# Kernel optimization log

Hardware: AMD Instinct MI355X
Metric: run time of the kernel (lower is better)

The kernel has to match this reference:

```python
import jax, jax.numpy as jnp
import numpy as np

B, T, NT = 256, 1024, 96  # batch, max seq len, num_tags (incl. start/end)


def setup_inputs() -> dict:
    key = jax.random.key(0)
    k1, k2, k3 = jax.random.split(key, 3)
    h = jax.random.normal(k1, (B, T, NT), dtype=jnp.float32)
    # lengths in [1, T]; force at least one full-length sequence so max_len == T
    lengths = jax.random.randint(k2, (B,), 1, T + 1).at[0].set(T)
    trans = jax.random.normal(k3, (NT, NT), dtype=jnp.float32)  # trans[to, from]
    return {"h": h, "lengths": lengths, "trans": trans}


def reference(h, lengths, trans):
    # CRF forward algorithm (log partition function), masked for variable lengths.
    Bb, Tt, nt = h.shape
    start_tag, end_tag = nt - 2, nt - 1  # start_tag=-2, end_tag=-1
    mask = jnp.arange(Tt)[None, :] < lengths[:, None]  # [B, T]

    score0 = jnp.full((Bb, nt), -10000.0, dtype=h.dtype).at[:, start_tag].set(0.0)

    def step(score, xs):
        h_t, m_t = xs  # h_t: [B, NT], m_t: [B]
        # score[b, j] (prev tag j) + trans[i, j] + emit h_t[b, i] -> [B, NT(i), NT(j)]
        s = score[:, None, :] + trans[None, :, :] + h_t[:, :, None]
        s = jax.nn.logsumexp(s, axis=2)  # [B, NT]
        score = jnp.where(m_t[:, None], s, score)
        return score, None

    score, _ = jax.lax.scan(step, score0, (jnp.swapaxes(h, 0, 1), mask.T))
    # transition into end tag, then final logsumexp over tags -> [B]
    return jax.nn.logsumexp(score + trans[end_tag][None, :], axis=1)
```

## Files before the change

### kernel.cpp

```cpp
#include <hip/hip_runtime.h>

#define Bb 256
#define Tt 1024
#define NT 96
#define PF 8

__global__ __attribute__((amdgpu_flat_work_group_size(256, 256),
                          amdgpu_waves_per_eu(1, 1)))
void crf_fwd_kernel(
    const float* __restrict__ h,
    const int*   __restrict__ lengths,
    const float* __restrict__ trans,
    float* __restrict__ out)
{
    const int b    = blockIdx.x;
    const int tid  = threadIdx.x;
    const int i    = tid >> 1;
    const int q    = tid & 1;
    const int L    = lengths[b];
    const bool active = (i < NT);
    const int wave = tid >> 6;

    __shared__ float p_lds[2][128];
    __shared__ float fin[4];

    float E[48];
    {
        const int ic = active ? i : 0;
        const float4* tr4 = reinterpret_cast<const float4*>(trans + ic * NT + q * 48);
        #pragma unroll
        for (int m = 0; m < 12; ++m) {
            const float4 t4 = tr4[m];
            E[4*m+0] = __expf(t4.x);
            E[4*m+1] = __expf(t4.y);
            E[4*m+2] = __expf(t4.z);
            E[4*m+3] = __expf(t4.w);
        }
    }
    asm volatile("" : "+v"(E[0]),  "+v"(E[1]),  "+v"(E[2]),  "+v"(E[3]),
                      "+v"(E[4]),  "+v"(E[5]),  "+v"(E[6]),  "+v"(E[7]),
                      "+v"(E[8]),  "+v"(E[9]),  "+v"(E[10]), "+v"(E[11]));
    asm volatile("" : "+v"(E[12]), "+v"(E[13]), "+v"(E[14]), "+v"(E[15]),
                      "+v"(E[16]), "+v"(E[17]), "+v"(E[18]), "+v"(E[19]),
                      "+v"(E[20]), "+v"(E[21]), "+v"(E[22]), "+v"(E[23]));
    asm volatile("" : "+v"(E[24]), "+v"(E[25]), "+v"(E[26]), "+v"(E[27]),
                      "+v"(E[28]), "+v"(E[29]), "+v"(E[30]), "+v"(E[31]),
                      "+v"(E[32]), "+v"(E[33]), "+v"(E[34]), "+v"(E[35]));
    asm volatile("" : "+v"(E[36]), "+v"(E[37]), "+v"(E[38]), "+v"(E[39]),
                      "+v"(E[40]), "+v"(E[41]), "+v"(E[42]), "+v"(E[43]),
                      "+v"(E[44]), "+v"(E[45]), "+v"(E[46]), "+v"(E[47]));

    if (tid < 128) p_lds[0][tid] = (tid == NT - 2) ? 1.0f : 0.0f;

    const float* hb  = h + (size_t)b * Tt * NT;
    const float* hld = active ? (hb + i) : hb;

    float hpA[PF], hpB[PF];
    #pragma unroll
    for (int k = 0; k < PF; ++k) hpA[k] = hld[(size_t)k * NT];
    #pragma unroll
    for (int k = 0; k < PF; ++k) hpB[k] = hld[(size_t)(PF + k) * NT];

    const float c  = 4.0f;
    const float Kc = __expf(-c);
    float M = 0.0f;
    float p_keep = 0.0f;

    __syncthreads();

    int cur = 0;

#define STEP(HREG, T_)                                                        \
    {                                                                         \
        const float p0 = p_lds[cur][0];                                       \
        const float4* pv = reinterpret_cast<const float4*>(p_lds[cur] + q*48);\
        float a0 = 0.f, a1 = 0.f, a2 = 0.f, a3 = 0.f;                         \
        _Pragma("unroll")                                                     \
        for (int m_ = 0; m_ < 12; ++m_) {                                     \
            const float4 p4 = pv[m_];                                         \
            a0 = fmaf(E[4*m_+0], p4.x, a0);                                   \
            a1 = fmaf(E[4*m_+1], p4.y, a1);                                   \
            a2 = fmaf(E[4*m_+2], p4.z, a2);                                   \
            a3 = fmaf(E[4*m_+3], p4.w, a3);                                   \
        }                                                                     \
        float v = (a0 + a1) + (a2 + a3);                                      \
        v += __shfl_xor(v, 1, 64);                                            \
        const float eh = __expf(HREG);                                        \
        const float u  = ((T_) == 0) ? 1.0f : Kc * __builtin_amdgcn_rcpf(p0); \
        const float w  = v * eh;                                              \
        const bool msk = ((T_) < L);                                          \
        const float pn = msk ? (w * u) : p_keep;                              \
        M -= msk ? __logf(u) : 0.0f;                                          \
        p_keep = pn;                                                          \
        if (active && q == 0) p_lds[cur ^ 1][i] = pn;                         \
        asm volatile("s_waitcnt lgkmcnt(0)" ::: "memory");                    \
        __builtin_amdgcn_s_barrier();                                         \
        asm volatile("" ::: "memory");                                        \
        cur ^= 1;                                                             \
    }

    for (int tb = 0; tb < Tt; tb += 2 * PF) {
        #pragma unroll
        for (int k = 0; k < PF; ++k) STEP(hpA[k], tb + k);

        #pragma unroll
        for (int m = 0; m < PF; ++m) {
            int tn = tb + 2 * PF + m; if (tn > Tt - 1) tn = Tt - 1;
            hpA[m] = hld[(size_t)tn * NT];
        }

        #pragma unroll
        for (int k = 0; k < PF; ++k) STEP(hpB[k], tb + PF + k);

        #pragma unroll
        for (int m = 0; m < PF; ++m) {
            int tn = tb + 3 * PF + m; if (tn > Tt - 1) tn = Tt - 1;
            hpB[m] = hld[(size_t)tn * NT];
        }
    }
#undef STEP

    float term = (active && q == 0) ? p_keep * __expf(trans[(NT - 1) * NT + i]) : 0.0f;
    #pragma unroll
    for (int s = 1; s < 64; s <<= 1) term += __shfl_xor(term, s, 64);
    if ((tid & 63) == 0) fin[wave] = term;
    __syncthreads();
    if (tid == 0) out[b] = M + __logf(fin[0] + fin[1] + fin[2] + fin[3]);
}

extern "C" void kernel_launch(void* const* d_in, const int* in_sizes, int n_in,
                              void* d_out, int out_size, void* d_ws, size_t ws_size,
                              hipStream_t stream) {
    const float* h       = (const float*)d_in[0];
    const int*   lengths = (const int*)d_in[1];
    const float* trans   = (const float*)d_in[2];
    float*       out     = (float*)d_out;
    (void)in_sizes; (void)n_in; (void)out_size; (void)d_ws; (void)ws_size;

    crf_fwd_kernel<<<Bb, 256, 0, stream>>>(h, lengths, trans, out);
}
```

Before: 381.3 us.

## Process two batch sequences per block to interleave independent recurrences

Each block now handles two sequences with 192 threads, sharing the exponentiated transition registers and interleaving two independent dot-product chains per step. The aim is to hide per-step LDS, shuffle and barrier latency of the serial recurrence with extra independent work. It halves the grid to 128 blocks, which leaves CUs idle, and it cuts prefetch depth to fit registers.

```diff
diff --git a/kernel.cpp b/kernel.cpp
--- a/kernel.cpp
+++ b/kernel.cpp
@@ -3,9 +3,9 @@
 #define Bb 256
 #define Tt 1024
 #define NT 96
-#define PF 8
+#define PF 4
 
-__global__ __attribute__((amdgpu_flat_work_group_size(256, 256),
+__global__ __attribute__((amdgpu_flat_work_group_size(192, 192),
                           amdgpu_waves_per_eu(1, 1)))
 void crf_fwd_kernel(
     const float* __restrict__ h,
@@ -13,21 +13,22 @@
     const float* __restrict__ trans,
     float* __restrict__ out)
 {
-    const int b    = blockIdx.x;
-    const int tid  = threadIdx.x;
-    const int i    = tid >> 1;
-    const int q    = tid & 1;
-    const int L    = lengths[b];
-    const bool active = (i < NT);
+    const int blk = blockIdx.x;
+    const int b0  = blk * 2, b1 = blk * 2 + 1;
+    const int tid = threadIdx.x;
+    const int i   = tid >> 1;
+    const int q   = tid & 1;
     const int wave = tid >> 6;
+    const int L0  = lengths[b0];
+    const int L1  = lengths[b1];
 
-    __shared__ float p_lds[2][128];
-    __shared__ float fin[4];
+    __shared__ float pl0[2][128];
+    __shared__ float pl1[2][128];
+    __shared__ float fin0[3], fin1[3];
 
     float E[48];
     {
-        const int ic = active ? i : 0;
-        const float4* tr4 = reinterpret_cast<const float4*>(trans + ic * NT + q * 48);
+        const float4* tr4 = reinterpret_cast<const float4*>(trans + i * NT + q * 48);
         #pragma unroll
         for (int m = 0; m < 12; ++m) {
             const float4 t4 = tr4[m];
@@ -50,49 +51,66 @@
                       "+v"(E[40]), "+v"(E[41]), "+v"(E[42]), "+v"(E[43]),
                       "+v"(E[44]), "+v"(E[45]), "+v"(E[46]), "+v"(E[47]));
 
-    if (tid < 128) p_lds[0][tid] = (tid == NT - 2) ? 1.0f : 0.0f;
+    if (tid < 128) {
+        const float v0 = (tid == NT - 2) ? 1.0f : 0.0f;
+        pl0[0][tid] = v0;
+        pl1[0][tid] = v0;
+    }
 
-    const float* hb  = h + (size_t)b * Tt * NT;
-    const float* hld = active ? (hb + i) : hb;
+    const float* h0 = h + (size_t)b0 * Tt * NT + i;
+    const float* h1 = h + (size_t)b1 * Tt * NT + i;
+    float hp0A[PF], hp0B[PF], hp1A[PF], hp1B[PF];
+    #pragma unroll
+    for (int k = 0; k < PF; ++k) {
+        hp0A[k] = h0[(size_t)k * NT];
+        hp1A[k] = h1[(size_t)k * NT];
+        hp0B[k] = h0[(size_t)(PF + k) * NT];
+        hp1B[k] = h1[(size_t)(PF + k) * NT];
+    }
 
-    float hpA[PF], hpB[PF];
-    #pragma unroll
-    for (int k = 0; k < PF; ++k) hpA[k] = hld[(size_t)k * NT];
-    #pragma unroll
-    for (int k = 0; k < PF; ++k) hpB[k] = hld[(size_t)(PF + k) * NT];
-
-    const float c  = 4.0f;
-    const float Kc = __expf(-c);
-    float M = 0.0f;
-    float p_keep = 0.0f;
+    const float Kc = __expf(-4.0f);
+    float M0 = 0.0f, M1 = 0.0f, pk0 = 0.0f, pk1 = 0.0f;
 
     __syncthreads();
 
     int cur = 0;
 
-#define STEP(HREG, T_)                                                        \
+#define STEP2(H0R, H1R, T_)                                                   \
     {                                                                         \
-        const float p0 = p_lds[cur][0];                                       \
-        const float4* pv = reinterpret_cast<const float4*>(p_lds[cur] + q*48);\
+        const float p00 = pl0[cur][0];                                        \
+        const float p10 = pl1[cur][0];                                        \
+        const float4* pv0 = reinterpret_cast<const float4*>(pl0[cur] + q*48); \
+        const float4* pv1 = reinterpret_cast<const float4*>(pl1[cur] + q*48); \
         float a0 = 0.f, a1 = 0.f, a2 = 0.f, a3 = 0.f;                         \
+        float c0 = 0.f, c1 = 0.f, c2 = 0.f, c3 = 0.f;                         \
         _Pragma("unroll")                                                     \
         for (int m_ = 0; m_ < 12; ++m_) {                                     \
-            const float4 p4 = pv[m_];                                         \
-            a0 = fmaf(E[4*m_+0], p4.x, a0);                                   \
-            a1 = fmaf(E[4*m_+1], p4.y, a1);                                   \
-            a2 = fmaf(E[4*m_+2], p4.z, a2);                                   \
-            a3 = fmaf(E[4*m_+3], p4.w, a3);                                   \
+            const float4 x4 = pv0[m_];                                        \
+            const float4 y4 = pv1[m_];                                        \
+            a0 = fmaf(E[4*m_+0], x4.x, a0);                                   \
+            a1 = fmaf(E[4*m_+1], x4.y, a1);                                   \
+            a2 = fmaf(E[4*m_+2], x4.z, a2);                                   \
+            a3 = fmaf(E[4*m_+3], x4.w, a3);                                   \
+            c0 = fmaf(E[4*m_+0], y4.x, c0);                                   \
+            c1 = fmaf(E[4*m_+1], y4.y, c1);                                   \
+            c2 = fmaf(E[4*m_+2], y4.z, c2);                                   \
+            c3 = fmaf(E[4*m_+3], y4.w, c3);                                   \
         }                                                                     \
-        float v = (a0 + a1) + (a2 + a3);                                      \
-        v += __shfl_xor(v, 1, 64);                                            \
-        const float eh = __expf(HREG);                                        \
-        const float u  = ((T_) == 0) ? 1.0f : Kc * __builtin_amdgcn_rcpf(p0); \
-        const float w  = v * eh;                                              \
-        const bool msk = ((T_) < L);                                          \
-        const float pn = msk ? (w * u) : p_keep;                              \
-        M -= msk ? __logf(u) : 0.0f;                                          \
-        p_keep = pn;                                                          \
-        if (active && q == 0) p_lds[cur ^ 1][i] = pn;                         \
+        float v0 = (a0 + a1) + (a2 + a3);                                     \
+        float v1 = (c0 + c1) + (c2 + c3);                                     \
+        v0 += __shfl_xor(v0, 1, 64);                                          \
+        v1 += __shfl_xor(v1, 1, 64);                                          \
+        const float u0 = ((T_) == 0) ? 1.0f : Kc * __builtin_amdgcn_rcpf(p00);\
+        const float u1 = ((T_) == 0) ? 1.0f : Kc * __builtin_amdgcn_rcpf(p10);\
+        const float w0 = v0 * __expf(H0R) * u0;                               \
+        const float w1 = v1 * __expf(H1R) * u1;                               \
+        const bool mk0 = ((T_) < L0);                                         \
+        const bool mk1 = ((T_) < L1);                                         \
+        pk0 = mk0 ? w0 : pk0;                                                 \
+        pk1 = mk1 ? w1 : pk1;                                                 \
+        M0 -= mk0 ? __logf(u0) : 0.0f;                                        \
+        M1 -= mk1 ? __logf(u1) : 0.0f;                                        \
+        if (q == 0) { pl0[cur ^ 1][i] = pk0; pl1[cur ^ 1][i] = pk1; }         \
         asm volatile("s_waitcnt lgkmcnt(0)" ::: "memory");                    \
         __builtin_amdgcn_s_barrier();                                         \
         asm volatile("" ::: "memory");                                        \
@@ -101,31 +119,41 @@
 
     for (int tb = 0; tb < Tt; tb += 2 * PF) {
         #pragma unroll
-        for (int k = 0; k < PF; ++k) STEP(hpA[k], tb + k);
+        for (int k = 0; k < PF; ++k) STEP2(hp0A[k], hp1A[k], tb + k);
 
         #pragma unroll
         for (int m = 0; m < PF; ++m) {
             int tn = tb + 2 * PF + m; if (tn > Tt - 1) tn = Tt - 1;
-            hpA[m] = hld[(size_t)tn * NT];
+            hp0A[m] = h0[(size_t)tn * NT];
+            hp1A[m] = h1[(size_t)tn * NT];
         }
 
         #pragma unroll
-        for (int k = 0; k < PF; ++k) STEP(hpB[k], tb + PF + k);
+        for (int k = 0; k < PF; ++k) STEP2(hp0B[k], hp1B[k], tb + PF + k);
 
         #pragma unroll
         for (int m = 0; m < PF; ++m) {
             int tn = tb + 3 * PF + m; if (tn > Tt - 1) tn = Tt - 1;
-            hpB[m] = hld[(size_t)tn * NT];
+            hp0B[m] = h0[(size_t)tn * NT];
+            hp1B[m] = h1[(size_t)tn * NT];
         }
     }
-#undef STEP
+#undef STEP2
 
-    float term = (active && q == 0) ? p_keep * __expf(trans[(NT - 1) * NT + i]) : 0.0f;
+    const float eT = __expf(trans[(NT - 1) * NT + i]);
+    float t0 = (q == 0) ? pk0 * eT : 0.0f;
+    float t1 = (q == 0) ? pk1 * eT : 0.0f;
     #pragma unroll
-    for (int s = 1; s < 64; s <<= 1) term += __shfl_xor(term, s, 64);
-    if ((tid & 63) == 0) fin[wave] = term;
+    for (int s = 1; s < 64; s <<= 1) {
+        t0 += __shfl_xor(t0, s, 64);
+        t1 += __shfl_xor(t1, s, 64);
+    }
+    if ((tid & 63) == 0) { fin0[wave] = t0; fin1[wave] = t1; }
     __syncthreads();
-    if (tid == 0) out[b] = M + __logf(fin[0] + fin[1] + fin[2] + fin[3]);
+    if (tid == 0) {
+        out[b0] = M0 + __logf(fin0[0] + fin0[1] + fin0[2]);
+        out[b1] = M1 + __logf(fin1[0] + fin1[1] + fin1[2]);
+    }
 }
 
 extern "C" void kernel_launch(void* const* d_in, const int* in_sizes, int n_in,
@@ -137,5 +165,5 @@
     float*       out     = (float*)d_out;
     (void)in_sizes; (void)n_in; (void)out_size; (void)d_ws; (void)ws_size;
 
-    crf_fwd_kernel<<<Bb, 256, 0, stream>>>(h, lengths, trans, out);
+    crf_fwd_kernel<<<Bb / 2, 192, 0, stream>>>(h, lengths, trans, out);
 }
```

After: 591.7 us. +55.2%, slower.
